# Kernel tuning notes

Measured on AMD Instinct MI355X. Metric: run time of the kernel, lower is better.

## Reference

```python
import jax, jax.numpy as jnp
import numpy as np

NUM_LAYERS = 24      # controller steps (architecture layers)
NUM_ACTIONS = 16
LSTM_SIZE = 2048
LSTM_NUM_LAYERS = 2


def setup_inputs() -> dict:
    key = jax.random.key(0)
    ks = jax.random.split(key, 7)
    H, A, L = LSTM_SIZE, NUM_ACTIONS, LSTM_NUM_LAYERS
    s = 0.05  # init scale to keep gates unsaturated
    return {
        "g_emb": jax.random.normal(ks[0], (1, H), jnp.float32) * s,
        "w_emb": jax.random.normal(ks[1], (A, H), jnp.float32) * s,
        "soft_w": jax.random.normal(ks[2], (H, A), jnp.float32) * s,
        "w_ih": jax.random.normal(ks[3], (L, 4 * H, H), jnp.float32) * s,
        "w_hh": jax.random.normal(ks[4], (L, 4 * H, H), jnp.float32) * s,
        "b_ih": jax.random.normal(ks[5], (L, 4 * H), jnp.float32) * s,
        "b_hh": jax.random.normal(ks[6], (L, 4 * H), jnp.float32) * s,
    }


def _controller(g_emb, w_emb, soft_w, w_ih, w_hh, b_ih, b_hh):
    H, L = LSTM_SIZE, LSTM_NUM_LAYERS
    sample_keys = jax.random.split(jax.random.key(42), NUM_LAYERS)

    def lstm_stack(x, h, c):
        # x: [1,H]; h, c: [L,1,H]. PyTorch gate order: i, f, g, o.
        h_new, c_new = [], []
        for l in range(L):
            gates = x @ w_ih[l].T + h[l] @ w_hh[l].T + b_ih[l] + b_hh[l]  # [1,4H]
            i_g, f_g, g_g, o_g = jnp.split(gates, 4, axis=-1)
            c_l = jax.nn.sigmoid(f_g) * c[l] + jax.nn.sigmoid(i_g) * jnp.tanh(g_g)
            h_l = jax.nn.sigmoid(o_g) * jnp.tanh(c_l)
            h_new.append(h_l)
            c_new.append(c_l)
            x = h_l
        return x, jnp.stack(h_new), jnp.stack(c_new)

    def step(carry, k):
        x, h, c = carry
        out, h, c = lstm_stack(x, h, c)          # out: [1,H]
        logits = (out @ soft_w)[0]               # [A]
        action = jax.random.categorical(k, logits)
        logp = jax.nn.log_softmax(logits)
        lp = logp[action]
        ent = -jnp.sum(jnp.exp(logp) * logp)
        x_next = w_emb[action][None, :]          # [1,H]
        return (x_next, h, c), (action, lp, ent)

    h0 = jnp.zeros((L, 1, H), g_emb.dtype)
    c0 = jnp.zeros((L, 1, H), g_emb.dtype)
    _, (actions, logprobs, entropies) = jax.lax.scan(step, (g_emb, h0, c0), sample_keys)
    return actions, logprobs, entropies


def reference(g_emb, w_emb, soft_w, w_ih, w_hh, b_ih, b_hh):
    # Returns (sampled architecture actions [num_layers] int,
    #          per-step log-probs [num_layers], per-step entropies [num_layers]).
    return _controller(g_emb, w_emb, soft_w, w_ih, w_hh, b_ih, b_hh)
```

## Files before the change

kernel.cpp:

```cpp
#include <hip/hip_runtime.h>
#include <math.h>

#define HD 2048
#define NACT 16
#define NSTEP 24
#define WL (4*HD*HD)
#define NIH (2*WL)

#define NWG 256
#define NTHR 512
#define NWG_FB 256
#define NTHR_FB 512

typedef float  nf4 __attribute__((ext_vector_type(4)));

__device__ __forceinline__ float ld_agent(const float* p) {
  return __hip_atomic_load(p, __ATOMIC_RELAXED, __HIP_MEMORY_SCOPE_AGENT);
}
__device__ __forceinline__ void st_agent(float* p, float v) {
  __hip_atomic_store(p, v, __ATOMIC_RELAXED, __HIP_MEMORY_SCOPE_AGENT);
}

__device__ __forceinline__ unsigned rotl32(unsigned v, int r) { return (v << r) | (v >> (32 - r)); }

__device__ __forceinline__ void threefry(unsigned k0, unsigned k1, unsigned x0, unsigned x1,
                                         unsigned& o0, unsigned& o1) {
  unsigned ks2 = k0 ^ k1 ^ 0x1BD11BDAu;
#define TFR(r) { x0 += x1; x1 = rotl32(x1, r); x1 ^= x0; }
  x0 += k0; x1 += k1;
  TFR(13) TFR(15) TFR(26) TFR(6)
  x0 += k1;  x1 += ks2 + 1u;
  TFR(17) TFR(29) TFR(16) TFR(24)
  x0 += ks2; x1 += k0 + 2u;
  TFR(13) TFR(15) TFR(26) TFR(6)
  x0 += k0;  x1 += k1 + 3u;
  TFR(17) TFR(29) TFR(16) TFR(24)
  x0 += k1;  x1 += ks2 + 4u;
  TFR(13) TFR(15) TFR(26) TFR(6)
  x0 += ks2; x1 += k0 + 5u;
#undef TFR
  o0 = x0; o1 = x1;
}

__device__ __forceinline__ float sigmoidf(float x) { return 1.0f / (1.0f + expf(-x)); }

__device__ __forceinline__ unsigned f2bf(float f) {
  unsigned u = __float_as_uint(f);
  return (u + 0x7fffu + ((u >> 16) & 1u)) >> 16;
}
#define BF_LO(u) __uint_as_float((u) << 16)
#define BF_HI(u) __uint_as_float((u) & 0xffff0000u)

__device__ void grid_bar(unsigned* flags, unsigned ep) {
  __syncthreads();
  if (threadIdx.x == 0) {
    __hip_atomic_store(&flags[blockIdx.x], ep, __ATOMIC_RELAXED, __HIP_MEMORY_SCOPE_AGENT);
  }
  if (threadIdx.x < 64) {
    const unsigned* my = flags + threadIdx.x * 4;
    long guard = 0;
    for (;;) {
      unsigned f0 = __hip_atomic_load(my + 0, __ATOMIC_RELAXED, __HIP_MEMORY_SCOPE_AGENT);
      unsigned f1 = __hip_atomic_load(my + 1, __ATOMIC_RELAXED, __HIP_MEMORY_SCOPE_AGENT);
      unsigned f2 = __hip_atomic_load(my + 2, __ATOMIC_RELAXED, __HIP_MEMORY_SCOPE_AGENT);
      unsigned f3 = __hip_atomic_load(my + 3, __ATOMIC_RELAXED, __HIP_MEMORY_SCOPE_AGENT);
      bool ok = (f0 >= ep) && (f1 >= ep) && (f2 >= ep) && (f3 >= ep);
      if (__all(ok)) break;
      if (++guard > 2000000L) break;
      __builtin_amdgcn_s_sleep(8);
    }
  }
  __syncthreads();
}

__device__ int sample_step(const float* __restrict__ h1g, const float* __restrict__ soft_w,
                           int t, float* lp_out, float* ent_out) {
  __shared__ float s_part[8][NACT];
  __shared__ float s_res[3];
  const int wave = threadIdx.x >> 6;
  const int lane = threadIdx.x & 63;

  float lg[NACT];
#pragma unroll
  for (int a = 0; a < NACT; ++a) lg[a] = 0.0f;
#pragma unroll
  for (int m = 0; m < 4; ++m) {
    int e = wave * 256 + m * 64 + lane;
    float hv = ld_agent(h1g + e);
    const float* sw = soft_w + (size_t)e * NACT;
    float4 r0 = *(const float4*)(sw);
    float4 r1 = *(const float4*)(sw + 4);
    float4 r2 = *(const float4*)(sw + 8);
    float4 r3 = *(const float4*)(sw + 12);
    lg[0]  += hv * r0.x; lg[1]  += hv * r0.y; lg[2]  += hv * r0.z; lg[3]  += hv * r0.w;
    lg[4]  += hv * r1.x; lg[5]  += hv * r1.y; lg[6]  += hv * r1.z; lg[7]  += hv * r1.w;
    lg[8]  += hv * r2.x; lg[9]  += hv * r2.y; lg[10] += hv * r2.z; lg[11] += hv * r2.w;
    lg[12] += hv * r3.x; lg[13] += hv * r3.y; lg[14] += hv * r3.z; lg[15] += hv * r3.w;
  }
#pragma unroll
  for (int off = 32; off > 0; off >>= 1) {
#pragma unroll
    for (int a = 0; a < NACT; ++a) lg[a] += __shfl_xor(lg[a], off, 64);
  }
  if (lane == 0) {
#pragma unroll
    for (int a = 0; a < NACT; ++a) s_part[wave][a] = lg[a];
  }
  __syncthreads();

  if (wave == 0 && lane < NACT) {
    float logit = 0.0f;
#pragma unroll
    for (int w = 0; w < 8; ++w) logit += s_part[w][lane];

    unsigned kt0, kt1, b0, b1;
    threefry(0u, 42u, 0u, (unsigned)t, kt0, kt1);
    threefry(kt0, kt1, 0u, (unsigned)lane, b0, b1);
    unsigned bits = b0 ^ b1;

    const float tiny = 1.17549435e-38f;
    float u = __uint_as_float((bits >> 9) | 0x3f800000u) - 1.0f;
    u = fmaxf(tiny, u + tiny);
    float gmb = -logf(-logf(u));
    float z = logit + gmb;

    int idx = lane; float zz = z;
#pragma unroll
    for (int off = 8; off > 0; off >>= 1) {
      float oz = __shfl_xor(zz, off, NACT);
      int   oi = __shfl_xor(idx, off, NACT);
      if (oz > zz || (oz == zz && oi < idx)) { zz = oz; idx = oi; }
    }
    float mx = logit;
#pragma unroll
    for (int off = 8; off > 0; off >>= 1) mx = fmaxf(mx, __shfl_xor(mx, off, NACT));
    float sh = logit - mx;
    float se = expf(sh);
#pragma unroll
    for (int off = 8; off > 0; off >>= 1) se += __shfl_xor(se, off, NACT);
    float lp = sh - logf(se);
    float term = expf(lp) * lp;
#pragma unroll
    for (int off = 8; off > 0; off >>= 1) term += __shfl_xor(term, off, NACT);
    float lp_sel = __shfl(lp, idx, NACT);
    if (lane == 0) { s_res[0] = (float)idx; s_res[1] = lp_sel; s_res[2] = -term; }
  }
  __syncthreads();
  int act = (int)s_res[0];
  *lp_out = s_res[1];
  *ent_out = s_res[2];
  return act;
}


__global__ void __launch_bounds__(256) conv_bf16(const float* __restrict__ src,
                                                 unsigned* __restrict__ dst) {
  size_t i = ((size_t)blockIdx.x * blockDim.x + threadIdx.x) * 8;
  const nf4* s4 = (const nf4*)(src + i);
  nf4 a = __builtin_nontemporal_load(s4);
  nf4 b = __builtin_nontemporal_load(s4 + 1);
  uint4 o;
  o.x = (f2bf(a.y) << 16) | f2bf(a.x);
  o.y = (f2bf(a.w) << 16) | f2bf(a.z);
  o.z = (f2bf(b.y) << 16) | f2bf(b.x);
  o.w = (f2bf(b.w) << 16) | f2bf(b.z);
  *(uint4*)(dst + i / 2) = o;
}

__device__ void layer_bf16(const unsigned* __restrict__ wiL, const unsigned* __restrict__ whL,
                           const float* __restrict__ bihL, const float* __restrict__ bhhL,
                           const float* __restrict__ x, bool x_is_shared_state,
                           const float* __restrict__ hin,
                           float* __restrict__ hout, float* __restrict__ c,
                           float* s_x, float* s_h) {
  const int tid = threadIdx.x;
#pragma unroll
  for (int r = 0; r < 4; ++r) {
    int e = tid + r * 512;
    s_x[e] = x_is_shared_state ? ld_agent(x + e) : x[e];
    s_h[e] = ld_agent(hin + e);
  }
  __syncthreads();

  const int wave = tid >> 6;
  const int lane = tid & 63;
  const int j = (int)blockIdx.x * 8 + wave;

  float4 xv[8], hv[8];
#pragma unroll
  for (int k = 0; k < 8; ++k) {
    int e = k * 256 + lane * 4;
    xv[k] = *(const float4*)(s_x + e);
    hv[k] = *(const float4*)(s_h + e);
  }

  float acc[4];
#pragma unroll
  for (int g = 0; g < 4; ++g) {
    const unsigned* wi = wiL + ((size_t)(g * HD + j) * HD >> 1);
    const unsigned* wh = whL + ((size_t)(g * HD + j) * HD >> 1);
    float si = 0.0f, sh2 = 0.0f;
#pragma unroll
    for (int k = 0; k < 8; ++k) {
      int e2 = k * 128 + lane * 2;
      uint2 qa = *(const uint2*)(wi + e2);
      uint2 qb = *(const uint2*)(wh + e2);
      si  += BF_LO(qa.x) * xv[k].x + BF_HI(qa.x) * xv[k].y;
      si  += BF_LO(qa.y) * xv[k].z + BF_HI(qa.y) * xv[k].w;
      sh2 += BF_LO(qb.x) * hv[k].x + BF_HI(qb.x) * hv[k].y;
      sh2 += BF_LO(qb.y) * hv[k].z + BF_HI(qb.y) * hv[k].w;
    }
    acc[g] = si + sh2;
  }
#pragma unroll
  for (int off = 32; off > 0; off >>= 1) {
#pragma unroll
    for (int g = 0; g < 4; ++g) acc[g] += __shfl_xor(acc[g], off, 64);
  }
  if (lane == 0) {
    float gi = acc[0] + bihL[j]          + bhhL[j];
    float gf = acc[1] + bihL[HD + j]     + bhhL[HD + j];
    float gg = acc[2] + bihL[2 * HD + j] + bhhL[2 * HD + j];
    float go = acc[3] + bihL[3 * HD + j] + bhhL[3 * HD + j];
    float cn = sigmoidf(gf) * c[j] + sigmoidf(gi) * tanhf(gg);
    c[j] = cn;
    st_agent(&hout[j], sigmoidf(go) * tanhf(cn));
  }
}

__global__ void __launch_bounds__(NTHR) ctrl2_kernel(
    const float* __restrict__ g_emb, const float* __restrict__ w_emb,
    const float* __restrict__ soft_w,
    const unsigned* __restrict__ wb_ih, const unsigned* __restrict__ wb_hh,
    const float* __restrict__ b_ih, const float* __restrict__ b_hh,
    float* __restrict__ out, float* __restrict__ state, unsigned* __restrict__ flags) {
  __shared__ float s_x[HD];
  __shared__ float s_h[HD];
  float* h0 = state;
  float* h1 = state + 2 * HD;
  float* c0 = state + 4 * HD;
  float* c1 = state + 5 * HD;

  if (threadIdx.x < 8) {
    int j = (int)blockIdx.x * 8 + (int)threadIdx.x;
    st_agent(&h0[j], 0.0f); st_agent(&h1[j], 0.0f);
    c0[j] = 0.0f; c1[j] = 0.0f;
  }
  unsigned ep = 1;
  grid_bar(flags, ep++);

  const unsigned* wi0 = wb_ih;             const unsigned* wh0 = wb_hh;
  const unsigned* wi1 = wb_ih + WL / 2;    const unsigned* wh1 = wb_hh + WL / 2;

  const float* x = g_emb;
  for (int t = 0; t < NSTEP; ++t) {
    int q = t & 1;
    layer_bf16(wi0, wh0, b_ih, b_hh, x, false,
               h0 + q * HD, h0 + (1 - q) * HD, c0, s_x, s_h);
    grid_bar(flags, ep++);
    layer_bf16(wi1, wh1, b_ih + 4 * HD, b_hh + 4 * HD,
               h0 + (1 - q) * HD, true,
               h1 + q * HD, h1 + (1 - q) * HD, c1, s_x, s_h);
    grid_bar(flags, ep++);
    float lp, en;
    int act = sample_step(h1 + (1 - q) * HD, soft_w, t, &lp, &en);
    if (blockIdx.x == 0 && threadIdx.x == 0) {
      out[t] = (float)act;
      out[NSTEP + t] = lp;
      out[2 * NSTEP + t] = en;
    }
    x = w_emb + (size_t)act * HD;
  }
}


__device__ void grid_bar_ctr(unsigned long long* ctr, unsigned long long target) {
  __syncthreads();
  if (threadIdx.x == 0) {
    __builtin_amdgcn_fence(__ATOMIC_SEQ_CST, "agent");
    __hip_atomic_fetch_add(ctr, 1ull, __ATOMIC_RELAXED, __HIP_MEMORY_SCOPE_AGENT);
    long guard = 0;
    while (__hip_atomic_load(ctr, __ATOMIC_RELAXED, __HIP_MEMORY_SCOPE_AGENT) < target &&
           guard < 20000000L) {
      __builtin_amdgcn_s_sleep(2);
      ++guard;
    }
    __builtin_amdgcn_fence(__ATOMIC_SEQ_CST, "agent");
  }
  __syncthreads();
}

__device__ int sample_step8(const float* __restrict__ h1g, const float* __restrict__ soft_w,
                            int t, float* lp_out, float* ent_out) {
  __shared__ float s_part[8][NACT];
  __shared__ float s_res[3];
  const int wave = threadIdx.x >> 6;
  const int lane = threadIdx.x & 63;

  float lg[NACT];
#pragma unroll
  for (int a = 0; a < NACT; ++a) lg[a] = 0.0f;
#pragma unroll
  for (int m = 0; m < 4; ++m) {
    int e = wave * 256 + m * 64 + lane;
    float hv = h1g[e];
    const float* sw = soft_w + (size_t)e * NACT;
    float4 r0 = *(const float4*)(sw);
    float4 r1 = *(const float4*)(sw + 4);
    float4 r2 = *(const float4*)(sw + 8);
    float4 r3 = *(const float4*)(sw + 12);
    lg[0]  += hv * r0.x; lg[1]  += hv * r0.y; lg[2]  += hv * r0.z; lg[3]  += hv * r0.w;
    lg[4]  += hv * r1.x; lg[5]  += hv * r1.y; lg[6]  += hv * r1.z; lg[7]  += hv * r1.w;
    lg[8]  += hv * r2.x; lg[9]  += hv * r2.y; lg[10] += hv * r2.z; lg[11] += hv * r2.w;
    lg[12] += hv * r3.x; lg[13] += hv * r3.y; lg[14] += hv * r3.z; lg[15] += hv * r3.w;
  }
#pragma unroll
  for (int off = 32; off > 0; off >>= 1) {
#pragma unroll
    for (int a = 0; a < NACT; ++a) lg[a] += __shfl_xor(lg[a], off, 64);
  }
  if (lane == 0) {
#pragma unroll
    for (int a = 0; a < NACT; ++a) s_part[wave][a] = lg[a];
  }
  __syncthreads();

  if (wave == 0 && lane < NACT) {
    float logit = 0.0f;
#pragma unroll
    for (int w = 0; w < 8; ++w) logit += s_part[w][lane];
    unsigned kt0, kt1, b0, b1;
    threefry(0u, 42u, 0u, (unsigned)t, kt0, kt1);
    threefry(kt0, kt1, 0u, (unsigned)lane, b0, b1);
    unsigned bits = b0 ^ b1;
    const float tiny = 1.17549435e-38f;
    float u = __uint_as_float((bits >> 9) | 0x3f800000u) - 1.0f;
    u = fmaxf(tiny, u + tiny);
    float gmb = -logf(-logf(u));
    float z = logit + gmb;
    int idx = lane; float zz = z;
#pragma unroll
    for (int off = 8; off > 0; off >>= 1) {
      float oz = __shfl_xor(zz, off, NACT);
      int   oi = __shfl_xor(idx, off, NACT);
      if (oz > zz || (oz == zz && oi < idx)) { zz = oz; idx = oi; }
    }
    float mx = logit;
#pragma unroll
    for (int off = 8; off > 0; off >>= 1) mx = fmaxf(mx, __shfl_xor(mx, off, NACT));
    float sh = logit - mx;
    float se = expf(sh);
#pragma unroll
    for (int off = 8; off > 0; off >>= 1) se += __shfl_xor(se, off, NACT);
    float lp = sh - logf(se);
    float term = expf(lp) * lp;
#pragma unroll
    for (int off = 8; off > 0; off >>= 1) term += __shfl_xor(term, off, NACT);
    float lp_sel = __shfl(lp, idx, NACT);
    if (lane == 0) { s_res[0] = (float)idx; s_res[1] = lp_sel; s_res[2] = -term; }
  }
  __syncthreads();
  int act = (int)s_res[0];
  *lp_out = s_res[1];
  *ent_out = s_res[2];
  return act;
}

__device__ void lstm_layer(const float* __restrict__ Wih, const float* __restrict__ Whh,
                           const float* __restrict__ bih, const float* __restrict__ bhh,
                           const float* __restrict__ x, const float* __restrict__ hin,
                           float* __restrict__ hout, float* __restrict__ c) {
  const int wave = threadIdx.x >> 6;
  const int lane = threadIdx.x & 63;
  const int j = (int)blockIdx.x * 8 + wave;

  float4 xv[8], hv[8];
#pragma unroll
  for (int k = 0; k < 8; ++k) {
    int e = k * 256 + lane * 4;
    xv[k] = *(const float4*)(x + e);
    hv[k] = *(const float4*)(hin + e);
  }
  float acc[4];
#pragma unroll
  for (int g = 0; g < 4; ++g) {
    const float* wi = Wih + (size_t)(g * HD + j) * HD;
    const float* wh = Whh + (size_t)(g * HD + j) * HD;
    float s = 0.0f;
#pragma unroll
    for (int k = 0; k < 8; ++k) {
      int e = k * 256 + lane * 4;
      float4 a4 = *(const float4*)(wi + e);
      float4 b4 = *(const float4*)(wh + e);
      s += a4.x * xv[k].x; s += a4.y * xv[k].y; s += a4.z * xv[k].z; s += a4.w * xv[k].w;
      s += b4.x * hv[k].x; s += b4.y * hv[k].y; s += b4.z * hv[k].z; s += b4.w * hv[k].w;
    }
    acc[g] = s;
  }
#pragma unroll
  for (int off = 32; off > 0; off >>= 1) {
#pragma unroll
    for (int g = 0; g < 4; ++g) acc[g] += __shfl_xor(acc[g], off, 64);
  }
  if (lane == 0) {
    float gi = acc[0] + bih[j]          + bhh[j];
    float gf = acc[1] + bih[HD + j]     + bhh[HD + j];
    float gg = acc[2] + bih[2 * HD + j] + bhh[2 * HD + j];
    float go = acc[3] + bih[3 * HD + j] + bhh[3 * HD + j];
    float cn = sigmoidf(gf) * c[j] + sigmoidf(gi) * tanhf(gg);
    c[j] = cn;
    hout[j] = sigmoidf(go) * tanhf(cn);
  }
}

__global__ void __launch_bounds__(NTHR_FB) ctrl_kernel(
    const float* __restrict__ g_emb, const float* __restrict__ w_emb,
    const float* __restrict__ soft_w, const float* __restrict__ w_ih,
    const float* __restrict__ w_hh, const float* __restrict__ b_ih,
    const float* __restrict__ b_hh, float* __restrict__ out, float* __restrict__ ws) {
  float* h0 = ws;
  float* h1 = ws + 2 * HD;
  float* c0 = ws + 4 * HD;
  float* c1 = ws + 5 * HD;
  unsigned long long* bar = (unsigned long long*)(ws + 6 * HD);

  if (threadIdx.x < 8) {
    int j = (int)blockIdx.x * 8 + (int)threadIdx.x;
    h0[j] = 0.0f; h1[j] = 0.0f; c0[j] = 0.0f; c1[j] = 0.0f;
  }
  unsigned long long ep = 1;
  grid_bar_ctr(bar, (ep++) * NWG_FB);

  const float* x = g_emb;
  for (int t = 0; t < NSTEP; ++t) {
    int q = t & 1;
    lstm_layer(w_ih, w_hh, b_ih, b_hh, x, h0 + q * HD, h0 + (1 - q) * HD, c0);
    grid_bar_ctr(bar, (ep++) * NWG_FB);
    lstm_layer(w_ih + WL, w_hh + WL, b_ih + 4 * HD, b_hh + 4 * HD,
               h0 + (1 - q) * HD, h1 + q * HD, h1 + (1 - q) * HD, c1);
    grid_bar_ctr(bar, (ep++) * NWG_FB);
    float lp, en;
    int act = sample_step8(h1 + (1 - q) * HD, soft_w, t, &lp, &en);
    if (blockIdx.x == 0 && threadIdx.x == 0) {
      out[t] = (float)act;
      out[NSTEP + t] = lp;
      out[2 * NSTEP + t] = en;
    }
    x = w_emb + (size_t)act * HD;
  }
}

__global__ void init_sync(unsigned* flags) {
  flags[threadIdx.x] = 0u;
}
__global__ void init_bar(unsigned long long* bar) { *bar = 0ull; }

extern "C" void kernel_launch(void* const* d_in, const int* in_sizes, int n_in,
                              void* d_out, int out_size, void* d_ws, size_t ws_size,
                              hipStream_t stream) {
  const float* g_emb  = (const float*)d_in[0];
  const float* w_emb  = (const float*)d_in[1];
  const float* soft_w = (const float*)d_in[2];
  const float* w_ih   = (const float*)d_in[3];
  const float* w_hh   = (const float*)d_in[4];
  const float* b_ih   = (const float*)d_in[5];
  const float* b_hh   = (const float*)d_in[6];

  const size_t wbytes = (size_t)NIH * 2 * sizeof(unsigned short);
  const size_t need = wbytes + (size_t)6 * HD * sizeof(float) + NWG * sizeof(unsigned) + 64;

  if (ws_size >= need) {
    unsigned* wb_ih = (unsigned*)d_ws;
    unsigned* wb_hh = wb_ih + NIH / 2;
    float* state = (float*)((char*)d_ws + wbytes);
    unsigned* flags = (unsigned*)(state + 6 * HD);

    hipLaunchKernelGGL(init_sync, dim3(1), dim3(NWG), 0, stream, flags);
    hipLaunchKernelGGL(conv_bf16, dim3(NIH / (256 * 8)), dim3(256), 0, stream, w_ih, wb_ih);
    hipLaunchKernelGGL(conv_bf16, dim3(NIH / (256 * 8)), dim3(256), 0, stream, w_hh, wb_hh);
    hipLaunchKernelGGL(ctrl2_kernel, dim3(NWG), dim3(NTHR), 0, stream,
                       g_emb, w_emb, soft_w, wb_ih, wb_hh, b_ih, b_hh,
                       (float*)d_out, state, flags);
  } else {
    float* ws = (float*)d_ws;
    unsigned long long* bar = (unsigned long long*)(ws + 6 * HD);
    hipLaunchKernelGGL(init_bar, dim3(1), dim3(1), 0, stream, bar);
    hipLaunchKernelGGL(ctrl_kernel, dim3(NWG_FB), dim3(NTHR_FB), 0, stream,
                       g_emb, w_emb, soft_w, w_ih, w_hh, b_ih, b_hh,
                       (float*)d_out, ws);
  }
}
```

Baseline: 1.020 ms.

## Prefetch next layer's bf16 weights into registers before grid barriers

Splits the LSTM layer routine into weight prefetch, x/h staging, and compute. Each wave now loads the next layer's weight slice (64 uint2 per lane) into registers before the grid barrier, so global weight fetches overlap barrier waiting and the sampling step. The cost is a much larger register footprint (about 128 VGPRs for the weights alone). The launch bounds hint of 2 blocks per CU may force spilling.

```diff
diff --git a/kernel.cpp b/kernel.cpp
--- a/kernel.cpp
+++ b/kernel.cpp
@@ -167,48 +167,54 @@
   *(uint4*)(dst + i / 2) = o;
 }
 
-__device__ void layer_bf16(const unsigned* __restrict__ wiL, const unsigned* __restrict__ whL,
-                           const float* __restrict__ bihL, const float* __restrict__ bhhL,
-                           const float* __restrict__ x, bool x_is_shared_state,
-                           const float* __restrict__ hin,
-                           float* __restrict__ hout, float* __restrict__ c,
-                           float* s_x, float* s_h) {
-  const int tid = threadIdx.x;
+__device__ __forceinline__ void prefetch_w(const unsigned* __restrict__ wiL,
+                                           const unsigned* __restrict__ whL,
+                                           int j, int lane,
+                                           uint2 A[4][8], uint2 B[4][8]) {
+#pragma unroll
+  for (int g = 0; g < 4; ++g) {
+    const unsigned* wi = wiL + ((size_t)(g * HD + j) * HD >> 1) + lane * 2;
+    const unsigned* wh = whL + ((size_t)(g * HD + j) * HD >> 1) + lane * 2;
+#pragma unroll
+    for (int k = 0; k < 8; ++k) {
+      A[g][k] = *(const uint2*)(wi + k * 128);
+      B[g][k] = *(const uint2*)(wh + k * 128);
+    }
+  }
+}
+
+__device__ __forceinline__ void stage_xh(const float* __restrict__ x, bool x_is_shared,
+                                         const float* __restrict__ hin,
+                                         float* s_x, float* s_h, int tid) {
 #pragma unroll
   for (int r = 0; r < 4; ++r) {
     int e = tid + r * 512;
-    s_x[e] = x_is_shared_state ? ld_agent(x + e) : x[e];
+    s_x[e] = x_is_shared ? ld_agent(x + e) : x[e];
     s_h[e] = ld_agent(hin + e);
   }
   __syncthreads();
-
-  const int wave = tid >> 6;
-  const int lane = tid & 63;
-  const int j = (int)blockIdx.x * 8 + wave;
-
-  float4 xv[8], hv[8];
-#pragma unroll
-  for (int k = 0; k < 8; ++k) {
-    int e = k * 256 + lane * 4;
-    xv[k] = *(const float4*)(s_x + e);
-    hv[k] = *(const float4*)(s_h + e);
-  }
-
+}
+
+__device__ __forceinline__ void layer_compute(const float* __restrict__ bihL,
+                                              const float* __restrict__ bhhL,
+                                              const float* s_x, const float* s_h,
+                                              float* __restrict__ hout, float* __restrict__ c,
+                                              int j, int lane,
+                                              const uint2 A[4][8], const uint2 B[4][8]) {
   float acc[4];
 #pragma unroll
   for (int g = 0; g < 4; ++g) {
-    const unsigned* wi = wiL + ((size_t)(g * HD + j) * HD >> 1);
-    const unsigned* wh = whL + ((size_t)(g * HD + j) * HD >> 1);
     float si = 0.0f, sh2 = 0.0f;
 #pragma unroll
     for (int k = 0; k < 8; ++k) {
-      int e2 = k * 128 + lane * 2;
-      uint2 qa = *(const uint2*)(wi + e2);
-      uint2 qb = *(const uint2*)(wh + e2);
-      si  += BF_LO(qa.x) * xv[k].x + BF_HI(qa.x) * xv[k].y;
-      si  += BF_LO(qa.y) * xv[k].z + BF_HI(qa.y) * xv[k].w;
-      sh2 += BF_LO(qb.x) * hv[k].x + BF_HI(qb.x) * hv[k].y;
-      sh2 += BF_LO(qb.y) * hv[k].z + BF_HI(qb.y) * hv[k].w;
+      float4 xv = *(const float4*)(s_x + k * 256 + lane * 4);
+      float4 hv = *(const float4*)(s_h + k * 256 + lane * 4);
+      uint2 qa = A[g][k];
+      uint2 qb = B[g][k];
+      si  += BF_LO(qa.x) * xv.x + BF_HI(qa.x) * xv.y;
+      si  += BF_LO(qa.y) * xv.z + BF_HI(qa.y) * xv.w;
+      sh2 += BF_LO(qb.x) * hv.x + BF_HI(qb.x) * hv.y;
+      sh2 += BF_LO(qb.y) * hv.z + BF_HI(qb.y) * hv.w;
     }
     acc[g] = si + sh2;
   }
@@ -228,7 +234,8 @@
   }
 }
 
-__global__ void __launch_bounds__(NTHR) ctrl2_kernel(
+__global__ void __launch_bounds__(NTHR, 2)
+ctrl2_kernel(
     const float* __restrict__ g_emb, const float* __restrict__ w_emb,
     const float* __restrict__ soft_w,
     const unsigned* __restrict__ wb_ih, const unsigned* __restrict__ wb_hh,
@@ -241,30 +248,40 @@
   float* c0 = state + 4 * HD;
   float* c1 = state + 5 * HD;
 
-  if (threadIdx.x < 8) {
-    int j = (int)blockIdx.x * 8 + (int)threadIdx.x;
-    st_agent(&h0[j], 0.0f); st_agent(&h1[j], 0.0f);
-    c0[j] = 0.0f; c1[j] = 0.0f;
-  }
+  const int tid  = threadIdx.x;
+  const int wave = tid >> 6;
+  const int lane = tid & 63;
+  const int j = (int)blockIdx.x * 8 + wave;
+
+  if (tid < 8) {
+    int jj = (int)blockIdx.x * 8 + tid;
+    st_agent(&h0[jj], 0.0f); st_agent(&h1[jj], 0.0f);
+    c0[jj] = 0.0f; c1[jj] = 0.0f;
+  }
+
+  const unsigned* wi0 = wb_ih;             const unsigned* wh0 = wb_hh;
+  const unsigned* wi1 = wb_ih + WL / 2;    const unsigned* wh1 = wb_hh + WL / 2;
+
+  uint2 A[4][8], B[4][8];
+  prefetch_w(wi0, wh0, j, lane, A, B);
   unsigned ep = 1;
   grid_bar(flags, ep++);
-
-  const unsigned* wi0 = wb_ih;             const unsigned* wh0 = wb_hh;
-  const unsigned* wi1 = wb_ih + WL / 2;    const unsigned* wh1 = wb_hh + WL / 2;
 
   const float* x = g_emb;
   for (int t = 0; t < NSTEP; ++t) {
     int q = t & 1;
-    layer_bf16(wi0, wh0, b_ih, b_hh, x, false,
-               h0 + q * HD, h0 + (1 - q) * HD, c0, s_x, s_h);
+    stage_xh(x, false, h0 + q * HD, s_x, s_h, tid);
+    layer_compute(b_ih, b_hh, s_x, s_h, h0 + (1 - q) * HD, c0, j, lane, A, B);
+    prefetch_w(wi1, wh1, j, lane, A, B);
     grid_bar(flags, ep++);
-    layer_bf16(wi1, wh1, b_ih + 4 * HD, b_hh + 4 * HD,
-               h0 + (1 - q) * HD, true,
-               h1 + q * HD, h1 + (1 - q) * HD, c1, s_x, s_h);
+    stage_xh(h0 + (1 - q) * HD, true, h1 + q * HD, s_x, s_h, tid);
+    layer_compute(b_ih + 4 * HD, b_hh + 4 * HD, s_x, s_h,
+                  h1 + (1 - q) * HD, c1, j, lane, A, B);
+    prefetch_w(wi0, wh0, j, lane, A, B);
     grid_bar(flags, ep++);
     float lp, en;
     int act = sample_step(h1 + (1 - q) * HD, soft_w, t, &lp, &en);
-    if (blockIdx.x == 0 && threadIdx.x == 0) {
+    if (blockIdx.x == 0 && tid == 0) {
       out[t] = (float)act;
       out[NSTEP + t] = lp;
       out[2 * NSTEP + t] = en;
```

Measured after the change: 2.440 ms. 2.39x slower.

## Replace grid barriers with per-element tagged hidden-state dataflow synchronization

Applied to the files above, without the earlier changes.

Drops the flag-based grid barriers between LSTM layers and steps. Each hidden value is now written as a 64-bit word holding the step tag and the float value, and consumers poll each element until its tag matches. Blocks can then proceed as soon as the data they need is ready, without waiting at a global barrier. The cost is doubled state storage, many more polling atomic loads per element, an extra init kernel for the tags, and reliance on spin-waits with a guard counter.

```diff
diff --git a/kernel.cpp b/kernel.cpp
--- a/kernel.cpp
+++ b/kernel.cpp
@@ -13,12 +13,25 @@
 #define NTHR_FB 512
 
 typedef float  nf4 __attribute__((ext_vector_type(4)));
-
-__device__ __forceinline__ float ld_agent(const float* p) {
+typedef unsigned long long u64;
+
+__device__ __forceinline__ u64 ld64_agent(const u64* p) {
   return __hip_atomic_load(p, __ATOMIC_RELAXED, __HIP_MEMORY_SCOPE_AGENT);
 }
-__device__ __forceinline__ void st_agent(float* p, float v) {
+__device__ __forceinline__ void st64_agent(u64* p, u64 v) {
   __hip_atomic_store(p, v, __ATOMIC_RELAXED, __HIP_MEMORY_SCOPE_AGENT);
+}
+
+__device__ __forceinline__ float poll_tag(const u64* a, unsigned tag) {
+  u64 v = ld64_agent(a);
+  if ((unsigned)(v >> 32) != tag) {
+    long g = 0;
+    do {
+      __builtin_amdgcn_s_sleep(1);
+      v = ld64_agent(a);
+    } while ((unsigned)(v >> 32) != tag && ++g < 1000000L);
+  }
+  return __uint_as_float((unsigned)v);
 }
 
 __device__ __forceinline__ unsigned rotl32(unsigned v, int r) { return (v << r) | (v >> (32 - r)); }
@@ -51,107 +64,6 @@
 #define BF_LO(u) __uint_as_float((u) << 16)
 #define BF_HI(u) __uint_as_float((u) & 0xffff0000u)
 
-__device__ void grid_bar(unsigned* flags, unsigned ep) {
-  __syncthreads();
-  if (threadIdx.x == 0) {
-    __hip_atomic_store(&flags[blockIdx.x], ep, __ATOMIC_RELAXED, __HIP_MEMORY_SCOPE_AGENT);
-  }
-  if (threadIdx.x < 64) {
-    const unsigned* my = flags + threadIdx.x * 4;
-    long guard = 0;
-    for (;;) {
-      unsigned f0 = __hip_atomic_load(my + 0, __ATOMIC_RELAXED, __HIP_MEMORY_SCOPE_AGENT);
-      unsigned f1 = __hip_atomic_load(my + 1, __ATOMIC_RELAXED, __HIP_MEMORY_SCOPE_AGENT);
-      unsigned f2 = __hip_atomic_load(my + 2, __ATOMIC_RELAXED, __HIP_MEMORY_SCOPE_AGENT);
-      unsigned f3 = __hip_atomic_load(my + 3, __ATOMIC_RELAXED, __HIP_MEMORY_SCOPE_AGENT);
-      bool ok = (f0 >= ep) && (f1 >= ep) && (f2 >= ep) && (f3 >= ep);
-      if (__all(ok)) break;
-      if (++guard > 2000000L) break;
-      __builtin_amdgcn_s_sleep(8);
-    }
-  }
-  __syncthreads();
-}
-
-__device__ int sample_step(const float* __restrict__ h1g, const float* __restrict__ soft_w,
-                           int t, float* lp_out, float* ent_out) {
-  __shared__ float s_part[8][NACT];
-  __shared__ float s_res[3];
-  const int wave = threadIdx.x >> 6;
-  const int lane = threadIdx.x & 63;
-
-  float lg[NACT];
-#pragma unroll
-  for (int a = 0; a < NACT; ++a) lg[a] = 0.0f;
-#pragma unroll
-  for (int m = 0; m < 4; ++m) {
-    int e = wave * 256 + m * 64 + lane;
-    float hv = ld_agent(h1g + e);
-    const float* sw = soft_w + (size_t)e * NACT;
-    float4 r0 = *(const float4*)(sw);
-    float4 r1 = *(const float4*)(sw + 4);
-    float4 r2 = *(const float4*)(sw + 8);
-    float4 r3 = *(const float4*)(sw + 12);
-    lg[0]  += hv * r0.x; lg[1]  += hv * r0.y; lg[2]  += hv * r0.z; lg[3]  += hv * r0.w;
-    lg[4]  += hv * r1.x; lg[5]  += hv * r1.y; lg[6]  += hv * r1.z; lg[7]  += hv * r1.w;
-    lg[8]  += hv * r2.x; lg[9]  += hv * r2.y; lg[10] += hv * r2.z; lg[11] += hv * r2.w;
-    lg[12] += hv * r3.x; lg[13] += hv * r3.y; lg[14] += hv * r3.z; lg[15] += hv * r3.w;
-  }
-#pragma unroll
-  for (int off = 32; off > 0; off >>= 1) {
-#pragma unroll
-    for (int a = 0; a < NACT; ++a) lg[a] += __shfl_xor(lg[a], off, 64);
-  }
-  if (lane == 0) {
-#pragma unroll
-    for (int a = 0; a < NACT; ++a) s_part[wave][a] = lg[a];
-  }
-  __syncthreads();
-
-  if (wave == 0 && lane < NACT) {
-    float logit = 0.0f;
-#pragma unroll
-    for (int w = 0; w < 8; ++w) logit += s_part[w][lane];
-
-    unsigned kt0, kt1, b0, b1;
-    threefry(0u, 42u, 0u, (unsigned)t, kt0, kt1);
-    threefry(kt0, kt1, 0u, (unsigned)lane, b0, b1);
-    unsigned bits = b0 ^ b1;
-
-    const float tiny = 1.17549435e-38f;
-    float u = __uint_as_float((bits >> 9) | 0x3f800000u) - 1.0f;
-    u = fmaxf(tiny, u + tiny);
-    float gmb = -logf(-logf(u));
-    float z = logit + gmb;
-
-    int idx = lane; float zz = z;
-#pragma unroll
-    for (int off = 8; off > 0; off >>= 1) {
-      float oz = __shfl_xor(zz, off, NACT);
-      int   oi = __shfl_xor(idx, off, NACT);
-      if (oz > zz || (oz == zz && oi < idx)) { zz = oz; idx = oi; }
-    }
-    float mx = logit;
-#pragma unroll
-    for (int off = 8; off > 0; off >>= 1) mx = fmaxf(mx, __shfl_xor(mx, off, NACT));
-    float sh = logit - mx;
-    float se = expf(sh);
-#pragma unroll
-    for (int off = 8; off > 0; off >>= 1) se += __shfl_xor(se, off, NACT);
-    float lp = sh - logf(se);
-    float term = expf(lp) * lp;
-#pragma unroll
-    for (int off = 8; off > 0; off >>= 1) term += __shfl_xor(term, off, NACT);
-    float lp_sel = __shfl(lp, idx, NACT);
-    if (lane == 0) { s_res[0] = (float)idx; s_res[1] = lp_sel; s_res[2] = -term; }
-  }
-  __syncthreads();
-  int act = (int)s_res[0];
-  *lp_out = s_res[1];
-  *ent_out = s_res[2];
-  return act;
-}
-
 
 __global__ void __launch_bounds__(256) conv_bf16(const float* __restrict__ src,
                                                  unsigned* __restrict__ dst) {
@@ -167,25 +79,38 @@
   *(uint4*)(dst + i / 2) = o;
 }
 
-__device__ void layer_bf16(const unsigned* __restrict__ wiL, const unsigned* __restrict__ whL,
-                           const float* __restrict__ bihL, const float* __restrict__ bhhL,
-                           const float* __restrict__ x, bool x_is_shared_state,
-                           const float* __restrict__ hin,
-                           float* __restrict__ hout, float* __restrict__ c,
-                           float* s_x, float* s_h) {
+__device__ void stage_l0(const float* __restrict__ x, const u64* __restrict__ th_hin,
+                         unsigned tag, float* s_x, float* s_h) {
   const int tid = threadIdx.x;
+  __syncthreads();
+  *(float4*)(s_x + tid * 4) = *(const float4*)(x + tid * 4);
 #pragma unroll
   for (int r = 0; r < 4; ++r) {
     int e = tid + r * 512;
-    s_x[e] = x_is_shared_state ? ld_agent(x + e) : x[e];
-    s_h[e] = ld_agent(hin + e);
-  }
-  __syncthreads();
-
-  const int wave = tid >> 6;
-  const int lane = tid & 63;
-  const int j = (int)blockIdx.x * 8 + wave;
-
+    s_h[e] = poll_tag(th_hin + e, tag);
+  }
+  __syncthreads();
+}
+
+__device__ void stage_l1(const u64* __restrict__ th_x, unsigned tagx,
+                         const u64* __restrict__ th_hin, unsigned tagh,
+                         float* s_x, float* s_h) {
+  const int tid = threadIdx.x;
+  __syncthreads();
+#pragma unroll
+  for (int r = 0; r < 4; ++r) {
+    int e = tid + r * 512;
+    s_x[e] = poll_tag(th_x + e, tagx);
+    s_h[e] = poll_tag(th_hin + e, tagh);
+  }
+  __syncthreads();
+}
+
+__device__ void layer_core(const unsigned* __restrict__ wiL, const unsigned* __restrict__ whL,
+                           const float* __restrict__ bihL, const float* __restrict__ bhhL,
+                           const float* s_x, const float* s_h,
+                           u64* __restrict__ th_out, unsigned otag,
+                           float* __restrict__ c, int j, int lane) {
   float4 xv[8], hv[8];
 #pragma unroll
   for (int k = 0; k < 8; ++k) {
@@ -224,8 +149,88 @@
     float go = acc[3] + bihL[3 * HD + j] + bhhL[3 * HD + j];
     float cn = sigmoidf(gf) * c[j] + sigmoidf(gi) * tanhf(gg);
     c[j] = cn;
-    st_agent(&hout[j], sigmoidf(go) * tanhf(cn));
-  }
+    float hval = sigmoidf(go) * tanhf(cn);
+    st64_agent(&th_out[j], ((u64)otag << 32) | (u64)__float_as_uint(hval));
+  }
+}
+
+__device__ int sample_from_lds(const float* s_h, const float* __restrict__ soft_w,
+                               int t, float* lp_out, float* ent_out) {
+  __shared__ float s_part[8][NACT];
+  __shared__ float s_res[3];
+  const int wave = threadIdx.x >> 6;
+  const int lane = threadIdx.x & 63;
+
+  float lg[NACT];
+#pragma unroll
+  for (int a = 0; a < NACT; ++a) lg[a] = 0.0f;
+#pragma unroll
+  for (int m = 0; m < 4; ++m) {
+    int e = wave * 256 + m * 64 + lane;
+    float hv = s_h[e];
+    const float* sw = soft_w + (size_t)e * NACT;
+    float4 r0 = *(const float4*)(sw);
+    float4 r1 = *(const float4*)(sw + 4);
+    float4 r2 = *(const float4*)(sw + 8);
+    float4 r3 = *(const float4*)(sw + 12);
+    lg[0]  += hv * r0.x; lg[1]  += hv * r0.y; lg[2]  += hv * r0.z; lg[3]  += hv * r0.w;
+    lg[4]  += hv * r1.x; lg[5]  += hv * r1.y; lg[6]  += hv * r1.z; lg[7]  += hv * r1.w;
+    lg[8]  += hv * r2.x; lg[9]  += hv * r2.y; lg[10] += hv * r2.z; lg[11] += hv * r2.w;
+    lg[12] += hv * r3.x; lg[13] += hv * r3.y; lg[14] += hv * r3.z; lg[15] += hv * r3.w;
+  }
+#pragma unroll
+  for (int off = 32; off > 0; off >>= 1) {
+#pragma unroll
+    for (int a = 0; a < NACT; ++a) lg[a] += __shfl_xor(lg[a], off, 64);
+  }
+  if (lane == 0) {
+#pragma unroll
+    for (int a = 0; a < NACT; ++a) s_part[wave][a] = lg[a];
+  }
+  __syncthreads();
+
+  if (wave == 0 && lane < NACT) {
+    float logit = 0.0f;
+#pragma unroll
+    for (int w = 0; w < 8; ++w) logit += s_part[w][lane];
+
+    unsigned kt0, kt1, b0, b1;
+    threefry(0u, 42u, 0u, (unsigned)t, kt0, kt1);
+    threefry(kt0, kt1, 0u, (unsigned)lane, b0, b1);
+    unsigned bits = b0 ^ b1;
+
+    const float tiny = 1.17549435e-38f;
+    float u = __uint_as_float((bits >> 9) | 0x3f800000u) - 1.0f;
+    u = fmaxf(tiny, u + tiny);
+    float gmb = -logf(-logf(u));
+    float z = logit + gmb;
+
+    int idx = lane; float zz = z;
+#pragma unroll
+    for (int off = 8; off > 0; off >>= 1) {
+      float oz = __shfl_xor(zz, off, NACT);
+      int   oi = __shfl_xor(idx, off, NACT);
+      if (oz > zz || (oz == zz && oi < idx)) { zz = oz; idx = oi; }
+    }
+    float mx = logit;
+#pragma unroll
+    for (int off = 8; off > 0; off >>= 1) mx = fmaxf(mx, __shfl_xor(mx, off, NACT));
+    float sh = logit - mx;
+    float se = expf(sh);
+#pragma unroll
+    for (int off = 8; off > 0; off >>= 1) se += __shfl_xor(se, off, NACT);
+    float lp = sh - logf(se);
+    float term = expf(lp) * lp;
+#pragma unroll
+    for (int off = 8; off > 0; off >>= 1) term += __shfl_xor(term, off, NACT);
+    float lp_sel = __shfl(lp, idx, NACT);
+    if (lane == 0) { s_res[0] = (float)idx; s_res[1] = lp_sel; s_res[2] = -term; }
+  }
+  __syncthreads();
+  int act = (int)s_res[0];
+  *lp_out = s_res[1];
+  *ent_out = s_res[2];
+  return act;
 }
 
 __global__ void __launch_bounds__(NTHR) ctrl2_kernel(
@@ -233,44 +238,55 @@
     const float* __restrict__ soft_w,
     const unsigned* __restrict__ wb_ih, const unsigned* __restrict__ wb_hh,
     const float* __restrict__ b_ih, const float* __restrict__ b_hh,
-    float* __restrict__ out, float* __restrict__ state, unsigned* __restrict__ flags) {
+    float* __restrict__ out, u64* __restrict__ th0, u64* __restrict__ th1,
+    float* __restrict__ cst) {
   __shared__ float s_x[HD];
   __shared__ float s_h[HD];
-  float* h0 = state;
-  float* h1 = state + 2 * HD;
-  float* c0 = state + 4 * HD;
-  float* c1 = state + 5 * HD;
-
-  if (threadIdx.x < 8) {
-    int j = (int)blockIdx.x * 8 + (int)threadIdx.x;
-    st_agent(&h0[j], 0.0f); st_agent(&h1[j], 0.0f);
-    c0[j] = 0.0f; c1[j] = 0.0f;
-  }
-  unsigned ep = 1;
-  grid_bar(flags, ep++);
+  float* c0 = cst;
+  float* c1 = cst + HD;
+
+  const int tid  = threadIdx.x;
+  const int wave = tid >> 6;
+  const int lane = tid & 63;
+  const int j = (int)blockIdx.x * 8 + wave;
+
+  if (tid < 8) {
+    int jj = (int)blockIdx.x * 8 + tid;
+    c0[jj] = 0.0f; c1[jj] = 0.0f;
+  }
 
   const unsigned* wi0 = wb_ih;             const unsigned* wh0 = wb_hh;
   const unsigned* wi1 = wb_ih + WL / 2;    const unsigned* wh1 = wb_hh + WL / 2;
 
   const float* x = g_emb;
   for (int t = 0; t < NSTEP; ++t) {
-    int q = t & 1;
-    layer_bf16(wi0, wh0, b_ih, b_hh, x, false,
-               h0 + q * HD, h0 + (1 - q) * HD, c0, s_x, s_h);
-    grid_bar(flags, ep++);
-    layer_bf16(wi1, wh1, b_ih + 4 * HD, b_hh + 4 * HD,
-               h0 + (1 - q) * HD, true,
-               h1 + q * HD, h1 + (1 - q) * HD, c1, s_x, s_h);
-    grid_bar(flags, ep++);
+    int s = t & 1, ps = s ^ 1;
+    stage_l0(x, th0 + ps * HD, (unsigned)t, s_x, s_h);
+    layer_core(wi0, wh0, b_ih, b_hh, s_x, s_h,
+               th0 + s * HD, (unsigned)(t + 1), c0, j, lane);
+    stage_l1(th0 + s * HD, (unsigned)(t + 1), th1 + ps * HD, (unsigned)t, s_x, s_h);
+    layer_core(wi1, wh1, b_ih + 4 * HD, b_hh + 4 * HD, s_x, s_h,
+               th1 + s * HD, (unsigned)(t + 1), c1, j, lane);
+    __syncthreads();
+#pragma unroll
+    for (int r = 0; r < 4; ++r) {
+      int e = tid + r * 512;
+      s_h[e] = poll_tag(th1 + s * HD + e, (unsigned)(t + 1));
+    }
+    __syncthreads();
     float lp, en;
-    int act = sample_step(h1 + (1 - q) * HD, soft_w, t, &lp, &en);
-    if (blockIdx.x == 0 && threadIdx.x == 0) {
+    int act = sample_from_lds(s_h, soft_w, t, &lp, &en);
+    if (blockIdx.x == 0 && tid == 0) {
       out[t] = (float)act;
       out[NSTEP + t] = lp;
       out[2 * NSTEP + t] = en;
     }
     x = w_emb + (size_t)act * HD;
   }
+}
+
+__global__ void __launch_bounds__(1024) init_tags(u64* th) {
+  th[(size_t)blockIdx.x * 1024 + threadIdx.x] = 0ull;
 }
 
 
@@ -450,9 +466,6 @@
   }
 }
 
-__global__ void init_sync(unsigned* flags) {
-  flags[threadIdx.x] = 0u;
-}
 __global__ void init_bar(unsigned long long* bar) { *bar = 0ull; }
 
 extern "C" void kernel_launch(void* const* d_in, const int* in_sizes, int n_in,
@@ -467,20 +480,22 @@
   const float* b_hh   = (const float*)d_in[6];
 
   const size_t wbytes = (size_t)NIH * 2 * sizeof(unsigned short);
-  const size_t need = wbytes + (size_t)6 * HD * sizeof(float) + NWG * sizeof(unsigned) + 64;
+  const size_t tagbytes = (size_t)8 * HD * sizeof(u64);
+  const size_t need = wbytes + tagbytes + (size_t)2 * HD * sizeof(float) + 64;
 
   if (ws_size >= need) {
     unsigned* wb_ih = (unsigned*)d_ws;
     unsigned* wb_hh = wb_ih + NIH / 2;
-    float* state = (float*)((char*)d_ws + wbytes);
-    unsigned* flags = (unsigned*)(state + 6 * HD);
-
-    hipLaunchKernelGGL(init_sync, dim3(1), dim3(NWG), 0, stream, flags);
+    u64* th0 = (u64*)((char*)d_ws + wbytes);
+    u64* th1 = th0 + 2 * HD;
+    float* cst = (float*)(th0 + 4 * HD);
+
+    hipLaunchKernelGGL(init_tags, dim3(4 * HD * 2 / 1024), dim3(1024), 0, stream, th0);
     hipLaunchKernelGGL(conv_bf16, dim3(NIH / (256 * 8)), dim3(256), 0, stream, w_ih, wb_ih);
     hipLaunchKernelGGL(conv_bf16, dim3(NIH / (256 * 8)), dim3(256), 0, stream, w_hh, wb_hh);
     hipLaunchKernelGGL(ctrl2_kernel, dim3(NWG), dim3(NTHR), 0, stream,
                        g_emb, w_emb, soft_w, wb_ih, wb_hh, b_ih, b_hh,
-                       (float*)d_out, state, flags);
+                       (float*)d_out, th0, th1, cst);
   } else {
     float* ws = (float*)d_ws;
     unsigned long long* bar = (unsigned long long*)(ws + 6 * HD);
```

After: 833.0 us (median of 2 runs). -18.4%, faster.
